# Optimization experiments

Measured on AMD Instinct MI355X. Metric: run time of the kernel, lower is better.

The kernel has to match this reference:

```python
import jax, jax.numpy as jnp
import numpy as np

N_BANDS = 128
RESOLUTION = 64
N_FRAMES = 128
N_SAMPLES = 32768
BATCH = 16


def setup_inputs() -> dict:
    key = jax.random.key(0)
    k1, k2 = jax.random.split(key)
    x = jax.random.normal(k1, (BATCH, N_BANDS, RESOLUTION), dtype=jnp.float32)
    # resonance buffer: linspace(0, 0.999, resolution) repeated over frames, cumprod over frames
    r = jnp.linspace(0.0, 0.999, RESOLUTION, dtype=jnp.float32)[:, None]
    resonance = jnp.cumprod(jnp.broadcast_to(r, (RESOLUTION, N_FRAMES)), axis=-1)
    # filter bank buffer (morlet in the original); random stand-in with same shape/scale
    filter_bank = jax.random.normal(k2, (1, N_BANDS, N_SAMPLES), dtype=jnp.float32) * 0.1
    return {"x": x, "resonance": resonance, "filter_bank": filter_bank}


def _linear_interp_weights(n_in: int, n_out: int):
    # PyTorch F.interpolate(mode='linear', align_corners=False)
    scale = n_in / n_out
    pos = (jnp.arange(n_out, dtype=jnp.float32) + 0.5) * scale - 0.5
    pos = jnp.clip(pos, 0.0, n_in - 1)
    i0 = jnp.floor(pos).astype(jnp.int32)
    i1 = jnp.minimum(i0 + 1, n_in - 1)
    w = pos - i0.astype(jnp.float32)
    return i0, i1, w


def reference(x, resonance, filter_bank):
    # softmax over resolution axis, mix resolution's resonance curves
    p = jax.nn.softmax(x, axis=-1)                      # (B, bands, resolution)
    frames = jnp.einsum('bcr,rf->bcf', p, resonance)    # (B, bands, n_frames)
    # linear upsample n_frames -> n_samples (align_corners=False)
    i0, i1, w = _linear_interp_weights(frames.shape[-1], N_SAMPLES)
    up = frames[..., i0] * (1.0 - w) + frames[..., i1] * w  # (B, bands, n_samples)
    # multiply by filter bank, mean over bands
    out = jnp.mean(up * filter_bank, axis=1, keepdims=True)  # (B, 1, n_samples)
    return out
```

## Files before the change

### kernel.cpp

```cpp
#include <hip/hip_runtime.h>

#define NB 16
#define NC 128
#define NR 64
#define NF 128
#define NS 32768
#define TS 64
#define CPAD 132

__global__ __launch_bounds__(64) void frames_kernel(
    const float* __restrict__ x,
    const float* __restrict__ resonance,
    float* __restrict__ framesT)
{
    const int row = blockIdx.x;
    const int r   = threadIdx.x;

    float xv = x[row * NR + r];

    float m = xv;
    #pragma unroll
    for (int off = 32; off >= 1; off >>= 1)
        m = fmaxf(m, __shfl_xor(m, off, 64));
    float e = __expf(xv - m);
    float ssum = e;
    #pragma unroll
    for (int off = 32; off >= 1; off >>= 1)
        ssum += __shfl_xor(ssum, off, 64);
    float p = e / ssum;

    __shared__ float psh[NR];
    psh[r] = p;
    __syncthreads();

    float acc0 = 0.f, acc1 = 0.f;
    #pragma unroll 8
    for (int rr = 0; rr < NR; ++rr) {
        float pr = psh[rr];
        acc0 = fmaf(pr, resonance[rr * NF + r],      acc0);
        acc1 = fmaf(pr, resonance[rr * NF + r + 64], acc1);
    }
    framesT[r        * (NB * NC) + row] = acc0;
    framesT[(r + 64) * (NB * NC) + row] = acc1;
}

__global__ __launch_bounds__(256) void mix_kernel(
    const float* __restrict__ framesT,
    const float* __restrict__ fbank,
    float* __restrict__ out)
{
    __shared__ float g0[NB * CPAD];
    __shared__ float g1[NB * CPAD];

    const int base = blockIdx.x * TS;
    const int tid  = threadIdx.x;

    float posb = (base + 0.5f) * (1.0f / 256.0f) - 0.5f;
    int i0 = (int)floorf(posb);
    i0 = i0 < 0 ? 0 : (i0 > NF - 1 ? NF - 1 : i0);
    const int i1 = (i0 + 1 < NF) ? i0 + 1 : NF - 1;

    {
        const float4* src0 = (const float4*)(framesT + (size_t)i0 * (NB * NC));
        const float4* src1 = (const float4*)(framesT + (size_t)i1 * (NB * NC));
        int bb = tid >> 5;
        int cc = (tid & 31) * 4;
        *(float4*)&g0[bb * CPAD + cc] = src0[tid];
        *(float4*)&g1[bb * CPAD + cc] = src1[tid];
        bb = (tid + 256) >> 5;
        cc = ((tid + 256) & 31) * 4;
        *(float4*)&g0[bb * CPAD + cc] = src0[tid + 256];
        *(float4*)&g1[bb * CPAD + cc] = src1[tid + 256];
    }
    __syncthreads();

    const int wv  = tid >> 6;
    const int l   = tid & 63;
    const int b   = l >> 2;
    const int sgl = l & 3;
    const int s0  = base + wv * 16 + sgl * 4;

    float w[4];
    #pragma unroll
    for (int j = 0; j < 4; ++j) {
        float p = (s0 + j + 0.5f) * (1.0f / 256.0f) - 0.5f;
        p = fminf(fmaxf(p, 0.f), (float)(NF - 1));
        w[j] = p - (float)i0;
    }

    float a0[4] = {0.f, 0.f, 0.f, 0.f};
    float a1[4] = {0.f, 0.f, 0.f, 0.f};
    const float* gb0 = &g0[b * CPAD];
    const float* gb1 = &g1[b * CPAD];

    #pragma unroll 8
    for (int c = 0; c < NC; ++c) {
        float4 fv = *(const float4*)&fbank[c * NS + s0];
        float q0 = gb0[c];
        float q1 = gb1[c];
        a0[0] = fmaf(q0, fv.x, a0[0]);
        a0[1] = fmaf(q0, fv.y, a0[1]);
        a0[2] = fmaf(q0, fv.z, a0[2]);
        a0[3] = fmaf(q0, fv.w, a0[3]);
        a1[0] = fmaf(q1, fv.x, a1[0]);
        a1[1] = fmaf(q1, fv.y, a1[1]);
        a1[2] = fmaf(q1, fv.z, a1[2]);
        a1[3] = fmaf(q1, fv.w, a1[3]);
    }

    const float inv = 1.0f / (float)NC;
    float4 r;
    r.x = ((1.f - w[0]) * a0[0] + w[0] * a1[0]) * inv;
    r.y = ((1.f - w[1]) * a0[1] + w[1] * a1[1]) * inv;
    r.z = ((1.f - w[2]) * a0[2] + w[2] * a1[2]) * inv;
    r.w = ((1.f - w[3]) * a0[3] + w[3] * a1[3]) * inv;
    *(float4*)&out[b * NS + s0] = r;
}

extern "C" void kernel_launch(void* const* d_in, const int* in_sizes, int n_in,
                              void* d_out, int out_size, void* d_ws, size_t ws_size,
                              hipStream_t stream) {
    const float* x    = (const float*)d_in[0];
    const float* res  = (const float*)d_in[1];
    const float* fbk  = (const float*)d_in[2];
    float* out        = (float*)d_out;
    float* framesT    = (float*)d_ws;

    frames_kernel<<<NB * NC, 64, 0, stream>>>(x, res, framesT);
    mix_kernel<<<NS / TS, 256, 0, stream>>>(framesT, fbk, out);
}
```

Baseline: 83.47 us.

## Split mix kernel over batch groups and channel quarters with XCD-aware tile mapping

The mix kernel now launches four times as many blocks, each handling four batch rows instead of sixteen. The 128 channels are split into four quarters across lanes and combined with cross-lane shuffles. Block indices are remapped so that neighbouring sample tiles land on the same XCD, which is meant to improve L2 reuse of filter-bank reads shared by the batch groups. The aim is more parallelism and occupancy, at the cost of reading the filter bank four times and extra shuffle reductions.

```diff
diff --git a/kernel.cpp b/kernel.cpp
--- a/kernel.cpp
+++ b/kernel.cpp
@@ -6,7 +6,8 @@
 #define NF 128
 #define NS 32768
 #define TS 64
-#define CPAD 132
+#define BPB 4
+#define QSTR 33
 
 __global__ __launch_bounds__(64) void frames_kernel(
     const float* __restrict__ x,
@@ -44,16 +45,23 @@
     framesT[(r + 64) * (NB * NC) + row] = acc1;
 }
 
-__global__ __launch_bounds__(256) void mix_kernel(
+__global__ __launch_bounds__(256, 4) void mix_kernel(
     const float* __restrict__ framesT,
     const float* __restrict__ fbank,
     float* __restrict__ out)
 {
-    __shared__ float g0[NB * CPAD];
-    __shared__ float g1[NB * CPAD];
+    __shared__ float g0[16 * QSTR];
+    __shared__ float g1[16 * QSTR];
 
-    const int base = blockIdx.x * TS;
-    const int tid  = threadIdx.x;
+    const int bid  = blockIdx.x;
+    const int xcd  = bid & 7;
+    const int j    = bid >> 3;
+    const int tile = xcd * 64 + (j & 63);
+    const int bg   = j >> 6;
+    const int b0   = bg * BPB;
+    const int base = tile * TS;
+
+    const int tid = threadIdx.x;
 
     float posb = (base + 0.5f) * (1.0f / 256.0f) - 0.5f;
     int i0 = (int)floorf(posb);
@@ -61,43 +69,44 @@
     const int i1 = (i0 + 1 < NF) ? i0 + 1 : NF - 1;
 
     {
-        const float4* src0 = (const float4*)(framesT + (size_t)i0 * (NB * NC));
-        const float4* src1 = (const float4*)(framesT + (size_t)i1 * (NB * NC));
-        int bb = tid >> 5;
-        int cc = (tid & 31) * 4;
-        *(float4*)&g0[bb * CPAD + cc] = src0[tid];
-        *(float4*)&g1[bb * CPAD + cc] = src1[tid];
-        bb = (tid + 256) >> 5;
-        cc = ((tid + 256) & 31) * 4;
-        *(float4*)&g0[bb * CPAD + cc] = src0[tid + 256];
-        *(float4*)&g1[bb * CPAD + cc] = src1[tid + 256];
+        const int t4   = tid & 127;
+        const int b    = t4 >> 5;
+        const int c4   = (t4 & 31) * 4;
+        const int A    = ((b << 2) + (c4 >> 5)) * QSTR + (c4 & 31);
+        const int fidx = (tid < 128) ? i0 : i1;
+        float* dst     = (tid < 128) ? g0 : g1;
+        float4 v = *(const float4*)&framesT[(size_t)fidx * (NB * NC) + b0 * NC + t4 * 4];
+        *(float4*)&dst[A] = v;
     }
     __syncthreads();
 
-    const int wv  = tid >> 6;
-    const int l   = tid & 63;
-    const int b   = l >> 2;
-    const int sgl = l & 3;
-    const int s0  = base + wv * 16 + sgl * 4;
+    const int wv = tid >> 6;
+    const int l  = tid & 63;
+    const int cq = l >> 4;
+    const int b  = (l >> 2) & 3;
+    const int g  = l & 3;
+    const int s0 = base + wv * 16 + g * 4;
 
     float w[4];
     #pragma unroll
-    for (int j = 0; j < 4; ++j) {
-        float p = (s0 + j + 0.5f) * (1.0f / 256.0f) - 0.5f;
+    for (int jj = 0; jj < 4; ++jj) {
+        float p = (s0 + jj + 0.5f) * (1.0f / 256.0f) - 0.5f;
         p = fminf(fmaxf(p, 0.f), (float)(NF - 1));
-        w[j] = p - (float)i0;
+        w[jj] = p - (float)i0;
     }
+
+    const float* q0p = &g0[((b << 2) + cq) * QSTR];
+    const float* q1p = &g1[((b << 2) + cq) * QSTR];
+    const float* fb  = &fbank[(size_t)(cq * 32) * NS + s0];
 
     float a0[4] = {0.f, 0.f, 0.f, 0.f};
     float a1[4] = {0.f, 0.f, 0.f, 0.f};
-    const float* gb0 = &g0[b * CPAD];
-    const float* gb1 = &g1[b * CPAD];
 
     #pragma unroll 8
-    for (int c = 0; c < NC; ++c) {
-        float4 fv = *(const float4*)&fbank[c * NS + s0];
-        float q0 = gb0[c];
-        float q1 = gb1[c];
+    for (int k = 0; k < 32; ++k) {
+        float4 fv = *(const float4*)&fb[(size_t)k * NS];
+        float q0 = q0p[k];
+        float q1 = q1p[k];
         a0[0] = fmaf(q0, fv.x, a0[0]);
         a0[1] = fmaf(q0, fv.y, a0[1]);
         a0[2] = fmaf(q0, fv.z, a0[2]);
@@ -108,13 +117,23 @@
         a1[3] = fmaf(q1, fv.w, a1[3]);
     }
 
-    const float inv = 1.0f / (float)NC;
-    float4 r;
-    r.x = ((1.f - w[0]) * a0[0] + w[0] * a1[0]) * inv;
-    r.y = ((1.f - w[1]) * a0[1] + w[1] * a1[1]) * inv;
-    r.z = ((1.f - w[2]) * a0[2] + w[2] * a1[2]) * inv;
-    r.w = ((1.f - w[3]) * a0[3] + w[3] * a1[3]) * inv;
-    *(float4*)&out[b * NS + s0] = r;
+    #pragma unroll
+    for (int jj = 0; jj < 4; ++jj) {
+        a0[jj] += __shfl_xor(a0[jj], 16, 64);
+        a0[jj] += __shfl_xor(a0[jj], 32, 64);
+        a1[jj] += __shfl_xor(a1[jj], 16, 64);
+        a1[jj] += __shfl_xor(a1[jj], 32, 64);
+    }
+
+    if (cq == 0) {
+        const float inv = 1.0f / (float)NC;
+        float4 r;
+        r.x = ((1.f - w[0]) * a0[0] + w[0] * a1[0]) * inv;
+        r.y = ((1.f - w[1]) * a0[1] + w[1] * a1[1]) * inv;
+        r.z = ((1.f - w[2]) * a0[2] + w[2] * a1[2]) * inv;
+        r.w = ((1.f - w[3]) * a0[3] + w[3] * a1[3]) * inv;
+        *(float4*)&out[(b0 + b) * NS + s0] = r;
+    }
 }
 
 extern "C" void kernel_launch(void* const* d_in, const int* in_sizes, int n_in,
@@ -127,5 +146,5 @@
     float* framesT    = (float*)d_ws;
 
     frames_kernel<<<NB * NC, 64, 0, stream>>>(x, res, framesT);
-    mix_kernel<<<NS / TS, 256, 0, stream>>>(framesT, fbk, out);
+    mix_kernel<<<(NS / TS) * (NB / BPB), 256, 0, stream>>>(framesT, fbk, out);
 }
```

Result: no change. 83.06 us (-0.5%).
